# Kernel tuning notes

Measured on AMD Instinct MI355X. Metric: run time of the kernel, lower is better.

Reference implementation:

```python
import jax, jax.numpy as jnp
import numpy as np

N, E, D, G, FP = 20000, 320000, 1280, 64, 65


def _glorot(k, shape):
    s = jnp.sqrt(6.0 / (shape[0] + shape[1])).astype(jnp.float32)
    return jax.random.uniform(k, shape, jnp.float32, -s, s)


def setup_inputs() -> dict:
    key = jax.random.key(0)
    ks = jax.random.split(key, 16)
    return {
        'x': jax.random.normal(ks[0], (N, D), jnp.float32),
        'edge_index': jax.random.randint(ks[1], (2, E), 0, N),
        'batch': jnp.sort(jax.random.randint(ks[2], (N,), 0, G)),
        'fp_x': jax.random.normal(ks[3], (G, FP), jnp.float32),
        'W1': _glorot(ks[4], (D, D)), 'b1': jnp.zeros((D,), jnp.float32),
        'W2': _glorot(ks[5], (D, 640)), 'b2': jnp.zeros((640,), jnp.float32),
        'W3': _glorot(ks[6], (640, 320)), 'b3': jnp.zeros((320,), jnp.float32),
        'Wg1': _glorot(ks[7], (320, 1024)), 'bg1': jnp.zeros((1024,), jnp.float32),
        'Wg2': _glorot(ks[8], (1024, 128)), 'bg2': jnp.zeros((128,), jnp.float32),
        'Wf1': _glorot(ks[9], (193, 1024)), 'bf1': jnp.zeros((1024,), jnp.float32),
        'Wf2': _glorot(ks[10], (1024, 512)), 'bf2': jnp.zeros((512,), jnp.float32),
        'Wo': _glorot(ks[11], (512, 1)), 'bo': jnp.zeros((1,), jnp.float32),
    }


def reference(x, edge_index, batch, fp_x, W1, b1, W2, b2, W3, b3,
              Wg1, bg1, Wg2, bg2, Wf1, bf1, Wf2, bf2, Wo, bo):
    n = x.shape[0]
    g = fp_x.shape[0]
    loop = jnp.arange(n)
    src = jnp.concatenate([edge_index[0], loop])  # self-loops added (GCNConv default)
    dst = jnp.concatenate([edge_index[1], loop])
    deg = jax.ops.segment_sum(jnp.ones_like(dst, x.dtype), dst, num_segments=n)
    dis = jnp.where(deg > 0, jax.lax.rsqrt(deg), 0.0)
    norm = dis[src] * dis[dst]  # D^-1/2 (A+I) D^-1/2 edge weights

    def gcn(h, W, b):
        h = h @ W                                  # transform first (PyG GCNConv)
        agg = jax.ops.segment_sum(h[src] * norm[:, None], dst, num_segments=n)
        return agg + b

    xt = jax.nn.relu(gcn(x, W1, b1))
    xt = jax.nn.relu(gcn(xt, W2, b2))
    xt = jax.nn.relu(gcn(xt, W3, b3))
    # global mean pool over graphs
    s = jax.ops.segment_sum(xt, batch, num_segments=g)
    cnt = jax.ops.segment_sum(jnp.ones((n,), xt.dtype), batch, num_segments=g)
    xt = s / jnp.maximum(cnt, 1.0)[:, None]
    # MLP head (dropout in eval mode -> identity)
    xt = jax.nn.relu(xt @ Wg1 + bg1)
    xt = xt @ Wg2 + bg2
    xc = jnp.concatenate([fp_x, xt], axis=1)       # [G, 65+128=193]
    xc = jax.nn.relu(xc @ Wf1 + bf1)
    xc = jax.nn.relu(xc @ Wf2 + bf2)
    return xc @ Wo + bo
```

## Files before the change

### kernel.cpp

```cpp
#include <hip/hip_runtime.h>
#include <hip/hip_bf16.h>

#define N_NODES 20000
#define NPAD    20224
#define N_EDGES 320000
#define NGRAPH  64
#define FPD     65

typedef __attribute__((ext_vector_type(8))) __bf16 bf16x8;
typedef __attribute__((ext_vector_type(4))) float floatx4;
typedef __attribute__((ext_vector_type(8))) ushort ushort8v;

__device__ inline float bf2f(ushort u) {
    union { unsigned int i; float f; } c; c.i = ((unsigned int)u) << 16; return c.f;
}
__device__ inline ushort f2bf(float v) {
    __hip_bfloat16 h = __float2bfloat16(v);
    return *(ushort*)&h;
}
__device__ __forceinline__ void gld_lds16(const ushort* g, ushort* l) {
    __builtin_amdgcn_global_load_lds(
        (const __attribute__((address_space(1))) unsigned int*)g,
        (__attribute__((address_space(3))) unsigned int*)l,
        16, 0, 0);
}

__global__ void count_in(const int* __restrict__ dst, int* cnt) {
    int e = blockIdx.x * blockDim.x + threadIdx.x;
    if (e < N_EDGES) atomicAdd(&cnt[dst[e]], 1);
}
__global__ __launch_bounds__(1024) void scan_offsets(const int* __restrict__ cnt,
                                                     int* __restrict__ off, int* __restrict__ cursor,
                                                     float* __restrict__ dis) {
    __shared__ int part[1024];
    int t = threadIdx.x;
    const int chunk = (N_NODES + 1023) / 1024;
    int lo = t * chunk, hi = min(lo + chunk, N_NODES);
    int s = 0;
    for (int i = lo; i < hi; ++i) s += (cnt[i] + 4) & ~3;
    part[t] = s;
    __syncthreads();
    for (int d = 1; d < 1024; d <<= 1) {
        int v = (t >= d) ? part[t - d] : 0;
        __syncthreads();
        part[t] += v;
        __syncthreads();
    }
    int base = part[t] - s;
    for (int i = lo; i < hi; ++i) {
        int c = cnt[i] + 1;
        off[i] = base; cursor[i] = base;
        dis[i] = rsqrtf((float)c);
        base += (c + 3) & ~3;
    }
    if (t == 1023) off[N_NODES] = part[1023];
}
__global__ __launch_bounds__(1024) void build_perm(const int* __restrict__ cnt,
                                                   int* __restrict__ perm) {
    __shared__ int hist[64];
    __shared__ int base[64];
    int t = threadIdx.x;
    if (t < 64) hist[t] = 0;
    __syncthreads();
    for (int i = t; i < N_NODES; i += 1024) {
        int g = ((cnt[i] + 4) & ~3) >> 2;
        atomicAdd(&hist[min(g, 63)], 1);
    }
    __syncthreads();
    if (t == 0) {
        int acc = 0;
        for (int b = 0; b < 64; ++b) { base[b] = acc; acc += hist[b]; }
    }
    __syncthreads();
    for (int i = t; i < N_NODES; i += 1024) {
        int g = ((cnt[i] + 4) & ~3) >> 2;
        int pos = atomicAdd(&base[min(g, 63)], 1);
        perm[pos] = i;
    }
}
__global__ void fill_csr(const int* __restrict__ src, const int* __restrict__ dst,
                         const float* __restrict__ dis, int* cursor,
                         int* __restrict__ esrc, float* __restrict__ ew) {
    int e = blockIdx.x * blockDim.x + threadIdx.x;
    if (e >= N_EDGES + N_NODES) return;
    int s, d; float w;
    if (e < N_EDGES) { s = src[e]; d = dst[e]; w = dis[s] * dis[d]; }
    else { s = d = e - N_EDGES; w = dis[s] * dis[s]; }
    int pos = atomicAdd(&cursor[d], 1);
    esrc[pos] = s; ew[pos] = w;
}
__global__ void fill_pad(const int* __restrict__ off, const int* __restrict__ cursor,
                         int* __restrict__ esrc, float* __restrict__ ew) {
    int i = blockIdx.x * blockDim.x + threadIdx.x;
    if (i >= N_NODES) return;
    int e1 = off[i + 1];
    for (int e = cursor[i]; e < e1; ++e) { esrc[e] = i; ew[e] = 0.f; }
}

__global__ __launch_bounds__(256) void prep_mega(
    const float* __restrict__ x, ushort* __restrict__ xbf,
    const float* __restrict__ W1, ushort* __restrict__ Wt1,
    const float* __restrict__ W2, ushort* __restrict__ Wt2,
    const float* __restrict__ W3, ushort* __restrict__ Wt3,
    const float* __restrict__ Wf1, float* __restrict__ Wf1p,
    const float* __restrict__ fp, float* __restrict__ xc,
    const int* __restrict__ batch, int* __restrict__ gstart)
{
    __shared__ float tsh[32][33];
    int b = blockIdx.x;
    if (b < 25000) {
        int idx = b * 256 + threadIdx.x;
        int n = idx / 320, f4 = idx % 320;
        float4 v = *(const float4*)(x + (size_t)n * 1280 + f4 * 4);
        ushort4 o;
        o.x = f2bf(v.x); o.y = f2bf(v.y); o.z = f2bf(v.z); o.w = f2bf(v.w);
        *(ushort4*)(xbf + (size_t)(f4 >> 4) * (NPAD * 64) + (size_t)n * 64 + (f4 & 15) * 4) = o;
        return;
    }
    b -= 25000;
    if (b < 2600) {
        const float* W; ushort* Wt; int Nc, KP, kt, nt;
        if (b < 1600)      { W = W1; Wt = Wt1; Nc = 1280; KP = 1344; kt = b % 40; nt = b / 40; }
        else if (b < 2400) { int b2 = b - 1600; W = W2; Wt = Wt2; Nc = 640; KP = 1344; kt = b2 % 40; nt = b2 / 40; }
        else               { int b2 = b - 2400; W = W3; Wt = Wt3; Nc = 320; KP = 704;  kt = b2 % 20; nt = b2 / 20; }
        int k0 = kt * 32, n0 = nt * 32;
        int tx = threadIdx.x & 31, ty = threadIdx.x >> 5;
        #pragma unroll
        for (int i = 0; i < 4; ++i)
            tsh[ty + i * 8][tx] = W[(size_t)(k0 + ty + i * 8) * Nc + n0 + tx];
        __syncthreads();
        #pragma unroll
        for (int i = 0; i < 4; ++i)
            Wt[(size_t)(n0 + ty + i * 8) * KP + k0 + tx] = f2bf(tsh[tx][ty + i * 8]);
        return;
    }
    b -= 2600;
    if (b < 832) {
        int idx = b * 256 + threadIdx.x;
        int k = idx / 1024;
        Wf1p[idx] = (k < 193) ? Wf1[idx] : 0.f;
        return;
    }
    b -= 832;
    if (b < 52) {
        int idx = b * 256 + threadIdx.x;
        if (idx < NGRAPH * 208) {
            int g = idx / 208, j = idx % 208;
            xc[idx] = (j < FPD) ? fp[g * FPD + j] : 0.f;
        }
        return;
    }
    b -= 52;
    {
        int n = b * 256 + threadIdx.x;
        if (n >= N_NODES) return;
        int bb = batch[n];
        int bp = (n == 0) ? -1 : batch[n - 1];
        for (int g = bp + 1; g <= bb; ++g) gstart[g] = n;
        if (n == N_NODES - 1)
            for (int g = bb + 1; g <= NGRAPH; ++g) gstart[g] = N_NODES;
    }
}


#define STAGE128(AsB, BsB, kt) do {                                                   \
    const ushort* Ak_ = A + (size_t)(kt) * (NPAD * 64);                               \
    const ushort* Bk_ = Bt + (size_t)(kt) * 64;                                       \
    _Pragma("unroll")                                                                 \
    for (int i_ = 0; i_ < 4; ++i_) {                                                  \
        int c_ = tid + i_ * 256;                                                      \
        int row_ = c_ >> 3, g_ = c_ & 7;                                              \
        gld_lds16(Ak_ + (size_t)(bm + row_) * 64 + (g_ ^ (row_ & 7)) * 8, &AsB[c_ * 8]); \
    }                                                                                 \
    _Pragma("unroll")                                                                 \
    for (int i_ = 0; i_ < 4; ++i_) {                                                  \
        int c_ = tid + i_ * 256;                                                      \
        int row_ = c_ >> 3, g_ = c_ & 7;                                              \
        gld_lds16(Bk_ + (size_t)(bn + row_) * KP + (g_ ^ (row_ & 7)) * 8, &BsB[c_ * 8]); \
    }                                                                                 \
} while (0)

#define COMPUTE128(AsB, BsB) do {                                                     \
    _Pragma("unroll")                                                                 \
    for (int ks = 0; ks < 2; ++ks) {                                                  \
        bf16x8 af[4], bfv[4];                                                         \
        _Pragma("unroll")                                                             \
        for (int t = 0; t < 4; ++t) {                                                 \
            int ra = wr * 64 + t * 16 + mr;                                           \
            af[t] = *(const bf16x8*)&AsB[ra * 64 + ((ks * 4 + quad) ^ (ra & 7)) * 8]; \
            int rb = wc * 64 + t * 16 + mr;                                           \
            bfv[t] = *(const bf16x8*)&BsB[rb * 64 + ((ks * 4 + quad) ^ (rb & 7)) * 8];\
        }                                                                             \
        _Pragma("unroll")                                                             \
        for (int tm = 0; tm < 4; ++tm)                                                \
            _Pragma("unroll")                                                         \
            for (int tn = 0; tn < 4; ++tn)                                            \
                acc[tm][tn] = __builtin_amdgcn_mfma_f32_16x16x32_bf16(af[tm], bfv[tn], acc[tm][tn], 0, 0, 0); \
    }                                                                                 \
} while (0)

__global__ __launch_bounds__(256) void gemm_bf16_128(
    const ushort* __restrict__ A, const ushort* __restrict__ Bt,
    ushort* __restrict__ C, int M, int K, int KP, int Nc, int nt, int total, int chunk)
{
    __shared__ ushort As0[128 * 64], As1[128 * 64];
    __shared__ ushort Bs0[128 * 64], Bs1[128 * 64];
    const int bi = blockIdx.x;
    const int tile = (bi & 7) * chunk + (bi >> 3);
    if (tile >= total) return;
    const int bm = (tile / nt) * 128, bn = (tile % nt) * 128;

    const int tid = threadIdx.x;
    const int wid = tid >> 6, lane = tid & 63;
    const int wr = wid >> 1, wc = wid & 1;
    const int quad = lane >> 4, mr = lane & 15;

    floatx4 acc[4][4];
    #pragma unroll
    for (int i = 0; i < 4; ++i)
        #pragma unroll
        for (int j = 0; j < 4; ++j)
            acc[i][j] = (floatx4){0.f, 0.f, 0.f, 0.f};

    const int NT = K >> 6;
    STAGE128(As0, Bs0, 0);
    __syncthreads();
    for (int kt = 0; kt < NT; kt += 2) {
        if (kt + 1 < NT) STAGE128(As1, Bs1, kt + 1);
        COMPUTE128(As0, Bs0);
        __syncthreads();
        if (kt + 1 < NT) {
            if (kt + 2 < NT) STAGE128(As0, Bs0, kt + 2);
            COMPUTE128(As1, Bs1);
            __syncthreads();
        }
    }

    ushort* Cc = C + (size_t)((bn >> 6) + wc) * (NPAD * 64);
    #pragma unroll
    for (int tm = 0; tm < 4; ++tm) {
        int rowb = bm + wr * 64 + tm * 16 + quad * 4;
        #pragma unroll
        for (int r = 0; r < 4; ++r) {
            int row = rowb + r;
            if (row < M) {
                #pragma unroll
                for (int tn = 0; tn < 4; ++tn)
                    Cc[(size_t)row * 64 + tn * 16 + mr] = f2bf(acc[tm][tn][r]);
            }
        }
    }
}

#define STAGE64(AsB, BsB, kt) do {                                                    \
    const ushort* Ak_ = A + (size_t)(kt) * (NPAD * 64);                               \
    const ushort* Bk_ = Bt + (size_t)(kt) * 64;                                       \
    _Pragma("unroll")                                                                 \
    for (int i_ = 0; i_ < 8; ++i_) {                                                  \
        int c_ = tid + i_ * 256;                                                      \
        int row_ = c_ >> 3, g_ = c_ & 7;                                              \
        gld_lds16(Ak_ + (size_t)(bm + row_) * 64 + (g_ ^ (row_ & 7)) * 8, &AsB[c_ * 8]); \
    }                                                                                 \
    _Pragma("unroll")                                                                 \
    for (int i_ = 0; i_ < 2; ++i_) {                                                  \
        int c_ = tid + i_ * 256;                                                      \
        int row_ = c_ >> 3, g_ = c_ & 7;                                              \
        gld_lds16(Bk_ + (size_t)(bn + row_) * KP + (g_ ^ (row_ & 7)) * 8, &BsB[c_ * 8]); \
    }                                                                                 \
} while (0)

#define COMPUTE64(AsB, BsB) do {                                                      \
    _Pragma("unroll")                                                                 \
    for (int ks = 0; ks < 2; ++ks) {                                                  \
        bf16x8 af[4], bfv[4];                                                         \
        _Pragma("unroll")                                                             \
        for (int t = 0; t < 4; ++t) {                                                 \
            int ra = wid * 64 + t * 16 + mr;                                          \
            af[t] = *(const bf16x8*)&AsB[ra * 64 + ((ks * 4 + quad) ^ (ra & 7)) * 8]; \
            int rb = t * 16 + mr;                                                     \
            bfv[t] = *(const bf16x8*)&BsB[rb * 64 + ((ks * 4 + quad) ^ (rb & 7)) * 8];\
        }                                                                             \
        _Pragma("unroll")                                                             \
        for (int tm = 0; tm < 4; ++tm)                                                \
            _Pragma("unroll")                                                         \
            for (int tn = 0; tn < 4; ++tn)                                            \
                acc[tm][tn] = __builtin_amdgcn_mfma_f32_16x16x32_bf16(af[tm], bfv[tn], acc[tm][tn], 0, 0, 0); \
    }                                                                                 \
} while (0)

__global__ __launch_bounds__(256) void gemm_bf16(
    const ushort* __restrict__ A, const ushort* __restrict__ Bt,
    ushort* __restrict__ C, int M, int K, int KP, int Nc, int nt, int total, int chunk)
{
    __shared__ ushort As0[256 * 64], As1[256 * 64];
    __shared__ ushort Bs0[64 * 64], Bs1[64 * 64];
    const int bi = blockIdx.x;
    const int tile = (bi & 7) * chunk + (bi >> 3);
    if (tile >= total) return;
    const int bm = (tile / nt) * 256, bn = (tile % nt) * 64;

    const int tid = threadIdx.x;
    const int wid = tid >> 6, lane = tid & 63;
    const int quad = lane >> 4, mr = lane & 15;

    floatx4 acc[4][4];
    #pragma unroll
    for (int i = 0; i < 4; ++i)
        #pragma unroll
        for (int j = 0; j < 4; ++j)
            acc[i][j] = (floatx4){0.f, 0.f, 0.f, 0.f};

    const int NT = K >> 6;
    STAGE64(As0, Bs0, 0);
    __syncthreads();
    for (int kt = 0; kt < NT; kt += 2) {
        if (kt + 1 < NT) STAGE64(As1, Bs1, kt + 1);
        COMPUTE64(As0, Bs0);
        __syncthreads();
        if (kt + 1 < NT) {
            if (kt + 2 < NT) STAGE64(As0, Bs0, kt + 2);
            COMPUTE64(As1, Bs1);
            __syncthreads();
        }
    }

    ushort* Cc = C + (size_t)(bn >> 6) * (NPAD * 64);
    #pragma unroll
    for (int tm = 0; tm < 4; ++tm) {
        int rowb = bm + wid * 64 + tm * 16 + quad * 4;
        #pragma unroll
        for (int r = 0; r < 4; ++r) {
            int row = rowb + r;
            if (row < M) {
                #pragma unroll
                for (int tn = 0; tn < 4; ++tn)
                    Cc[(size_t)row * 64 + tn * 16 + mr] = f2bf(acc[tm][tn][r]);
            }
        }
    }
}

static inline void launch_gemm(const ushort* A, const ushort* Bt, ushort* C,
                               int M, int K, int KP, int Nc, hipStream_t stream) {
    if (Nc % 128 == 0) {
        int mt = (M + 127) / 128, nt = Nc / 128;
        int total = mt * nt;
        int chunk = (total + 7) / 8;
        gemm_bf16_128<<<8 * chunk, 256, 0, stream>>>(A, Bt, C, M, K, KP, Nc, nt, total, chunk);
    } else {
        int mt = (M + 255) / 256, nt = Nc / 64;
        int total = mt * nt;
        int chunk = (total + 7) / 8;
        gemm_bf16<<<8 * chunk, 256, 0, stream>>>(A, Bt, C, M, K, KP, Nc, nt, total, chunk);
    }
}

template<int TPN>
__global__ __launch_bounds__(256) void gather_tiled(
    const ushort* __restrict__ h, const int* __restrict__ off,
    const int* __restrict__ esrc, const float* __restrict__ ew,
    const float* __restrict__ bias, ushort* __restrict__ out_bf,
    float* __restrict__ out_f32, const int* __restrict__ perm,
    int wbf, int wf32, int nchunks, int nbpc, int cpx)
{
    constexpr int NPB = 256 / TPN;
    const int bi = blockIdx.x;
    const int t2 = (bi & 7) * cpx + (bi >> 3);
    if (t2 >= nchunks * nbpc) return;
    const int c = t2 / nbpc, nb = t2 - c * nbpc;
    const int tid = threadIdx.x;
    const int g = tid / TPN, t = tid % TPN;
    const int np = nb * NPB + g;
    if (np >= N_NODES) return;
    const int n = perm[np];

    const ushort* hc = h + (size_t)c * (NPAD * 64) + t * 8;
    float acc[8];
    #pragma unroll
    for (int j = 0; j < 8; ++j) acc[j] = 0.f;

    const int e0 = off[n], e1 = off[n + 1];
    int4   s4 = *(const int4*)(esrc + e0);
    float4 w4 = *(const float4*)(ew + e0);
    ushort8v v0 = *(const ushort8v*)(hc + (size_t)s4.x * 64);
    ushort8v v1 = *(const ushort8v*)(hc + (size_t)s4.y * 64);
    ushort8v v2 = *(const ushort8v*)(hc + (size_t)s4.z * 64);
    ushort8v v3 = *(const ushort8v*)(hc + (size_t)s4.w * 64);
    for (int e = e0 + 4; e < e1; e += 4) {
        int4   s4n = *(const int4*)(esrc + e);
        float4 w4n = *(const float4*)(ew + e);
        ushort8v u0 = *(const ushort8v*)(hc + (size_t)s4n.x * 64);
        ushort8v u1 = *(const ushort8v*)(hc + (size_t)s4n.y * 64);
        ushort8v u2 = *(const ushort8v*)(hc + (size_t)s4n.z * 64);
        ushort8v u3 = *(const ushort8v*)(hc + (size_t)s4n.w * 64);
        #pragma unroll
        for (int j = 0; j < 8; ++j)
            acc[j] += w4.x * bf2f(v0[j]) + w4.y * bf2f(v1[j])
                    + w4.z * bf2f(v2[j]) + w4.w * bf2f(v3[j]);
        v0 = u0; v1 = u1; v2 = u2; v3 = u3; w4 = w4n;
    }
    #pragma unroll
    for (int j = 0; j < 8; ++j)
        acc[j] += w4.x * bf2f(v0[j]) + w4.y * bf2f(v1[j])
                + w4.z * bf2f(v2[j]) + w4.w * bf2f(v3[j]);

    const int fb = c * 64 + t * 8;
    float4 b0 = *(const float4*)(bias + fb);
    float4 b1 = *(const float4*)(bias + fb + 4);
    float r[8];
    r[0] = fmaxf(acc[0] + b0.x, 0.f); r[1] = fmaxf(acc[1] + b0.y, 0.f);
    r[2] = fmaxf(acc[2] + b0.z, 0.f); r[3] = fmaxf(acc[3] + b0.w, 0.f);
    r[4] = fmaxf(acc[4] + b1.x, 0.f); r[5] = fmaxf(acc[5] + b1.y, 0.f);
    r[6] = fmaxf(acc[6] + b1.z, 0.f); r[7] = fmaxf(acc[7] + b1.w, 0.f);
    if (wbf) {
        ushort8v o;
        #pragma unroll
        for (int j = 0; j < 8; ++j) o[j] = f2bf(r[j]);
        *(ushort8v*)(out_bf + (size_t)c * (NPAD * 64) + (size_t)n * 64 + t * 8) = o;
    }
    if (wf32) {
        *(float4*)(out_f32 + (size_t)n * (nchunks * 64) + fb)     = make_float4(r[0], r[1], r[2], r[3]);
        *(float4*)(out_f32 + (size_t)n * (nchunks * 64) + fb + 4) = make_float4(r[4], r[5], r[6], r[7]);
    }
}

static inline void launch_gather(const ushort* h, const int* off, const int* esrc,
                                 const float* ew, const float* bias, ushort* out_bf,
                                 float* out_f32, const int* perm,
                                 int wbf, int wf32, int nchunks, hipStream_t stream) {
    constexpr int TPN = 8;
    constexpr int NPB = 256 / TPN;
    const int nbpc = (N_NODES + NPB - 1) / NPB;
    const int total = nchunks * nbpc;
    const int cpx = (total + 7) / 8;
    gather_tiled<TPN><<<8 * cpx, 256, 0, stream>>>(
        h, off, esrc, ew, bias, out_bf, out_f32, perm, wbf, wf32, nchunks, nbpc, cpx);
}

__global__ __launch_bounds__(320) void pool_partial(
    const float* __restrict__ x, const int* __restrict__ gstart, float* __restrict__ pool)
{
    int g = blockIdx.x, q = blockIdx.y;
    int t = threadIdx.x;
    int s = gstart[g], e = gstart[g + 1], len = e - s;
    int lo = s + (len * q) / 4, hi = s + (len * (q + 1)) / 4;
    float a0 = 0.f, a1 = 0.f, a2 = 0.f, a3 = 0.f;
    int n = lo;
    for (; n + 3 < hi; n += 4) {
        a0 += x[(size_t)(n + 0) * 320 + t];
        a1 += x[(size_t)(n + 1) * 320 + t];
        a2 += x[(size_t)(n + 2) * 320 + t];
        a3 += x[(size_t)(n + 3) * 320 + t];
    }
    for (; n < hi; ++n) a0 += x[(size_t)n * 320 + t];
    float acc = (a0 + a1) + (a2 + a3);
    if (hi > lo) atomicAdd(&pool[g * 320 + t], acc);
}

template<int K, int SPLIT, int RELU, int SCALE>
__global__ __launch_bounds__(256) void head_gemm_sk(
    const float* __restrict__ in, int istride,
    const float* __restrict__ W, const float* __restrict__ b,
    float* __restrict__ out, int M, int Nc, int ostride, int ooff,
    const int* __restrict__ gs)
{
    constexpr int KQ = K / SPLIT;
    int idx = blockIdx.x * blockDim.x + threadIdx.x;
    int oi = idx / SPLIT, r = idx % SPLIT;
    if (oi >= M * Nc) return;
    int m = oi / Nc, c = oi % Nc;
    const float* ip = in + (size_t)m * istride + r * KQ;
    const float* wp = W + (size_t)r * KQ * Nc + c;
    float a0 = 0.f, a1 = 0.f, a2 = 0.f, a3 = 0.f;
    #pragma unroll
    for (int k = 0; k < KQ; k += 4) {
        float4 v = *(const float4*)(ip + k);
        a0 += v.x * wp[(size_t)(k + 0) * Nc];
        a1 += v.y * wp[(size_t)(k + 1) * Nc];
        a2 += v.z * wp[(size_t)(k + 2) * Nc];
        a3 += v.w * wp[(size_t)(k + 3) * Nc];
    }
    float s = (a0 + a1) + (a2 + a3);
    #pragma unroll
    for (int o = 1; o < SPLIT; o <<= 1) s += __shfl_xor(s, o, 64);
    if (r == 0) {
        if (SCALE) {
            float len = (float)(gs[m + 1] - gs[m]);
            s *= 1.f / fmaxf(len, 1.f);
        }
        s += b[c];
        out[(size_t)m * ostride + ooff + c] = RELU ? fmaxf(s, 0.f) : s;
    }
}

__global__ __launch_bounds__(256) void head_out(
    const float* __restrict__ f2, const float* __restrict__ Wo,
    const float* __restrict__ bo, float* __restrict__ out)
{
    int m = blockIdx.x;
    int t = threadIdx.x;
    float2 v = *(const float2*)(f2 + (size_t)m * 512 + t * 2);
    float2 w = *(const float2*)(Wo + t * 2);
    float s = v.x * w.x + v.y * w.y;
    #pragma unroll
    for (int o = 32; o > 0; o >>= 1) s += __shfl_down(s, o, 64);
    __shared__ float ps[4];
    if ((t & 63) == 0) ps[t >> 6] = s;
    __syncthreads();
    if (t == 0) out[m] = ps[0] + ps[1] + ps[2] + ps[3] + bo[0];
}

extern "C" void kernel_launch(void* const* d_in, const int* in_sizes, int n_in,
                              void* d_out, int out_size, void* d_ws, size_t ws_size,
                              hipStream_t stream) {
    const float* x    = (const float*)d_in[0];
    const int*   eidx = (const int*)d_in[1];
    const int*   batch= (const int*)d_in[2];
    const float* fp_x = (const float*)d_in[3];
    const float* W1 = (const float*)d_in[4];  const float* b1 = (const float*)d_in[5];
    const float* W2 = (const float*)d_in[6];  const float* b2 = (const float*)d_in[7];
    const float* W3 = (const float*)d_in[8];  const float* b3 = (const float*)d_in[9];
    const float* Wg1= (const float*)d_in[10]; const float* bg1= (const float*)d_in[11];
    const float* Wg2= (const float*)d_in[12]; const float* bg2= (const float*)d_in[13];
    const float* Wf1= (const float*)d_in[14]; const float* bf1= (const float*)d_in[15];
    const float* Wf2= (const float*)d_in[16]; const float* bf2= (const float*)d_in[17];
    const float* Wo = (const float*)d_in[18]; const float* bo = (const float*)d_in[19];
    float* out = (float*)d_out;

    const int* src = eidx;
    const int* dst = eidx + N_EDGES;

    char* p = (char*)d_ws;
    float* dis   = (float*)p;  p += 20480 * 4;
    int*   cntI  = (int*)p;    p += 20480 * 4;
    int*   off   = (int*)p;    p += 20480 * 4;
    int*   cursor= (int*)p;    p += 20480 * 4;
    int*   perm  = (int*)p;    p += 20480 * 4;
    int*   gstart= (int*)p;    p += 128 * 4;
    int*   esrc  = (int*)p;    p += 402432 * 4;
    float* ew    = (float*)p;  p += 402432 * 4;
    ushort* xbf  = (ushort*)p; p += (size_t)NPAD * 1280 * 2;
    ushort* hbf  = (ushort*)p; p += (size_t)NPAD * 1280 * 2;
    ushort* abf  = (ushort*)p; p += (size_t)NPAD * 1280 * 2;
    float* a3f   = (float*)p;  p += (size_t)N_NODES * 320 * 4;
    ushort* Wt1  = (ushort*)p; p += (size_t)1280 * 1344 * 2;
    ushort* Wt2  = (ushort*)p; p += (size_t)640 * 1344 * 2;
    ushort* Wt3  = (ushort*)p; p += (size_t)320 * 704 * 2;
    float* pool  = (float*)p;  p += NGRAPH * 320 * 4;
    float* m1    = (float*)p;  p += NGRAPH * 1024 * 4;
    float* xc    = (float*)p;  p += NGRAPH * 208 * 4;
    float* f1    = (float*)p;  p += NGRAPH * 1024 * 4;
    float* f2    = (float*)p;  p += NGRAPH * 512 * 4;
    float* Wf1p  = (float*)p;  p += 208 * 1024 * 4;

    hipMemsetAsync(cntI, 0, N_NODES * 4, stream);
    hipMemsetAsync(pool, 0, NGRAPH * 320 * 4, stream);

    prep_mega<<<25000 + 2600 + 832 + 52 + 79, 256, 0, stream>>>(
        x, xbf, W1, Wt1, W2, Wt2, W3, Wt3, Wf1, Wf1p, fp_x, xc, batch, gstart);

    count_in<<<(N_EDGES + 255) / 256, 256, 0, stream>>>(dst, cntI);
    build_perm<<<1, 1024, 0, stream>>>(cntI, perm);
    scan_offsets<<<1, 1024, 0, stream>>>(cntI, off, cursor, dis);
    fill_csr<<<(N_EDGES + N_NODES + 255) / 256, 256, 0, stream>>>(src, dst, dis, cursor, esrc, ew);
    fill_pad<<<(N_NODES + 255) / 256, 256, 0, stream>>>(off, cursor, esrc, ew);

    launch_gemm(xbf, Wt1, hbf, N_NODES, 1280, 1344, 1280, stream);
    launch_gather(hbf, off, esrc, ew, b1, abf, (float*)nullptr, perm, 1, 0, 20, stream);
    launch_gemm(abf, Wt2, hbf, N_NODES, 1280, 1344, 640, stream);
    launch_gather(hbf, off, esrc, ew, b2, abf, (float*)nullptr, perm, 1, 0, 10, stream);
    launch_gemm(abf, Wt3, hbf, N_NODES, 640, 704, 320, stream);
    launch_gather(hbf, off, esrc, ew, b3, (ushort*)nullptr, a3f, perm, 0, 1, 5, stream);

    pool_partial<<<dim3(NGRAPH, 4), 320, 0, stream>>>(a3f, gstart, pool);

    head_gemm_sk<320, 4, 1, 1><<<(NGRAPH * 1024 * 4 + 255) / 256, 256, 0, stream>>>(
        pool, 320, Wg1, bg1, m1, NGRAPH, 1024, 1024, 0, gstart);
    head_gemm_sk<1024, 8, 0, 0><<<(NGRAPH * 128 * 8 + 255) / 256, 256, 0, stream>>>(
        m1, 1024, Wg2, bg2, xc, NGRAPH, 128, 208, FPD, (const int*)nullptr);
    head_gemm_sk<208, 4, 1, 0><<<(NGRAPH * 1024 * 4 + 255) / 256, 256, 0, stream>>>(
        xc, 208, Wf1p, bf1, f1, NGRAPH, 1024, 1024, 0, (const int*)nullptr);
    head_gemm_sk<1024, 8, 1, 0><<<(NGRAPH * 512 * 8 + 255) / 256, 256, 0, stream>>>(
        f1, 1024, Wf2, bf2, f2, NGRAPH, 512, 512, 0, (const int*)nullptr);
    head_out<<<NGRAPH, 256, 0, stream>>>(f2, Wo, bo, out);
}
```

Before: 659.5 us.

## Replace double-buffered 128x128 GEMM with single-buffered 256x128 tile

The 128x128 bf16 GEMM, which used double-buffered LDS, is replaced by a 256x128 tile kernel in which each wave computes 64x128 outputs with a 4x8 accumulator array. This raises arithmetic intensity per LDS load and halves the number of M tiles. In exchange it drops the LDS double buffering, so loads and MFMA compute no longer overlap, and it uses more accumulator registers per thread, which can lower occupancy. It also launches fewer blocks, which may underfill the CUs when Nc is small.

```diff
diff --git a/kernel.cpp b/kernel.cpp
--- a/kernel.cpp
+++ b/kernel.cpp
@@ -162,91 +162,79 @@
     }
 }
 
-
-#define STAGE128(AsB, BsB, kt) do {                                                   \
-    const ushort* Ak_ = A + (size_t)(kt) * (NPAD * 64);                               \
-    const ushort* Bk_ = Bt + (size_t)(kt) * 64;                                       \
-    _Pragma("unroll")                                                                 \
-    for (int i_ = 0; i_ < 4; ++i_) {                                                  \
-        int c_ = tid + i_ * 256;                                                      \
-        int row_ = c_ >> 3, g_ = c_ & 7;                                              \
-        gld_lds16(Ak_ + (size_t)(bm + row_) * 64 + (g_ ^ (row_ & 7)) * 8, &AsB[c_ * 8]); \
-    }                                                                                 \
-    _Pragma("unroll")                                                                 \
-    for (int i_ = 0; i_ < 4; ++i_) {                                                  \
-        int c_ = tid + i_ * 256;                                                      \
-        int row_ = c_ >> 3, g_ = c_ & 7;                                              \
-        gld_lds16(Bk_ + (size_t)(bn + row_) * KP + (g_ ^ (row_ & 7)) * 8, &BsB[c_ * 8]); \
-    }                                                                                 \
-} while (0)
-
-#define COMPUTE128(AsB, BsB) do {                                                     \
-    _Pragma("unroll")                                                                 \
-    for (int ks = 0; ks < 2; ++ks) {                                                  \
-        bf16x8 af[4], bfv[4];                                                         \
-        _Pragma("unroll")                                                             \
-        for (int t = 0; t < 4; ++t) {                                                 \
-            int ra = wr * 64 + t * 16 + mr;                                           \
-            af[t] = *(const bf16x8*)&AsB[ra * 64 + ((ks * 4 + quad) ^ (ra & 7)) * 8]; \
-            int rb = wc * 64 + t * 16 + mr;                                           \
-            bfv[t] = *(const bf16x8*)&BsB[rb * 64 + ((ks * 4 + quad) ^ (rb & 7)) * 8];\
-        }                                                                             \
-        _Pragma("unroll")                                                             \
-        for (int tm = 0; tm < 4; ++tm)                                                \
-            _Pragma("unroll")                                                         \
-            for (int tn = 0; tn < 4; ++tn)                                            \
-                acc[tm][tn] = __builtin_amdgcn_mfma_f32_16x16x32_bf16(af[tm], bfv[tn], acc[tm][tn], 0, 0, 0); \
-    }                                                                                 \
-} while (0)
-
-__global__ __launch_bounds__(256) void gemm_bf16_128(
+__global__ __launch_bounds__(256) void gemm_bf16_256x128(
     const ushort* __restrict__ A, const ushort* __restrict__ Bt,
     ushort* __restrict__ C, int M, int K, int KP, int Nc, int nt, int total, int chunk)
 {
-    __shared__ ushort As0[128 * 64], As1[128 * 64];
-    __shared__ ushort Bs0[128 * 64], Bs1[128 * 64];
+    __shared__ ushort As[256 * 64];
+    __shared__ ushort Bs[128 * 64];
     const int bi = blockIdx.x;
     const int tile = (bi & 7) * chunk + (bi >> 3);
     if (tile >= total) return;
-    const int bm = (tile / nt) * 128, bn = (tile % nt) * 128;
+    const int bm = (tile / nt) * 256, bn = (tile % nt) * 128;
 
     const int tid = threadIdx.x;
     const int wid = tid >> 6, lane = tid & 63;
-    const int wr = wid >> 1, wc = wid & 1;
     const int quad = lane >> 4, mr = lane & 15;
 
-    floatx4 acc[4][4];
+    floatx4 acc[4][8];
     #pragma unroll
     for (int i = 0; i < 4; ++i)
         #pragma unroll
-        for (int j = 0; j < 4; ++j)
+        for (int j = 0; j < 8; ++j)
             acc[i][j] = (floatx4){0.f, 0.f, 0.f, 0.f};
 
-    const int NT = K >> 6;
-    STAGE128(As0, Bs0, 0);
-    __syncthreads();
-    for (int kt = 0; kt < NT; kt += 2) {
-        if (kt + 1 < NT) STAGE128(As1, Bs1, kt + 1);
-        COMPUTE128(As0, Bs0);
+    for (int k0 = 0; k0 < K; k0 += 64) {
+        const ushort* Ak = A + (size_t)(k0 >> 6) * (NPAD * 64);
+        #pragma unroll
+        for (int i = 0; i < 8; ++i) {
+            int c = tid + i * 256;
+            int row = c >> 3, g = c & 7;
+            gld_lds16(Ak + (size_t)(bm + row) * 64 + (g ^ (row & 7)) * 8, &As[c * 8]);
+        }
+        #pragma unroll
+        for (int i = 0; i < 4; ++i) {
+            int c = tid + i * 256;
+            int row = c >> 3, g = c & 7;
+            gld_lds16(Bt + (size_t)(bn + row) * KP + k0 + (g ^ (row & 7)) * 8, &Bs[c * 8]);
+        }
         __syncthreads();
-        if (kt + 1 < NT) {
-            if (kt + 2 < NT) STAGE128(As0, Bs0, kt + 2);
-            COMPUTE128(As1, Bs1);
-            __syncthreads();
-        }
-    }
-
-    ushort* Cc = C + (size_t)((bn >> 6) + wc) * (NPAD * 64);
+
+        #pragma unroll
+        for (int ks = 0; ks < 2; ++ks) {
+            bf16x8 af[4], bfv[8];
+            #pragma unroll
+            for (int t = 0; t < 4; ++t) {
+                int ra = wid * 64 + t * 16 + mr;
+                af[t] = *(const bf16x8*)&As[ra * 64 + ((ks * 4 + quad) ^ (ra & 7)) * 8];
+            }
+            #pragma unroll
+            for (int t = 0; t < 8; ++t) {
+                int rb = t * 16 + mr;
+                bfv[t] = *(const bf16x8*)&Bs[rb * 64 + ((ks * 4 + quad) ^ (rb & 7)) * 8];
+            }
+            #pragma unroll
+            for (int tm = 0; tm < 4; ++tm)
+                #pragma unroll
+                for (int tn = 0; tn < 8; ++tn)
+                    acc[tm][tn] = __builtin_amdgcn_mfma_f32_16x16x32_bf16(af[tm], bfv[tn], acc[tm][tn], 0, 0, 0);
+        }
+        __syncthreads();
+    }
+
+    const int cb = bn >> 6;
     #pragma unroll
     for (int tm = 0; tm < 4; ++tm) {
-        int rowb = bm + wr * 64 + tm * 16 + quad * 4;
+        int rowb = bm + wid * 64 + tm * 16 + quad * 4;
         #pragma unroll
         for (int r = 0; r < 4; ++r) {
             int row = rowb + r;
             if (row < M) {
                 #pragma unroll
-                for (int tn = 0; tn < 4; ++tn)
-                    Cc[(size_t)row * 64 + tn * 16 + mr] = f2bf(acc[tm][tn][r]);
+                for (int tn = 0; tn < 8; ++tn) {
+                    ushort* Cc = C + (size_t)(cb + (tn >> 2)) * (NPAD * 64);
+                    Cc[(size_t)row * 64 + (tn & 3) * 16 + mr] = f2bf(acc[tm][tn][r]);
+                }
             }
         }
     }
@@ -343,10 +331,10 @@
 static inline void launch_gemm(const ushort* A, const ushort* Bt, ushort* C,
                                int M, int K, int KP, int Nc, hipStream_t stream) {
     if (Nc % 128 == 0) {
-        int mt = (M + 127) / 128, nt = Nc / 128;
+        int mt = (M + 255) / 256, nt = Nc / 128;
         int total = mt * nt;
         int chunk = (total + 7) / 8;
-        gemm_bf16_128<<<8 * chunk, 256, 0, stream>>>(A, Bt, C, M, K, KP, Nc, nt, total, chunk);
+        gemm_bf16_256x128<<<8 * chunk, 256, 0, stream>>>(A, Bt, C, M, K, KP, Nc, nt, total, chunk);
     } else {
         int mt = (M + 255) / 256, nt = Nc / 64;
         int total = mt * nt;
```

Result: slower. 742.7 us (+12.6%).
